# Kernel tuning notes

Hardware: AMD Instinct MI355X
Metric: run time of the kernel (lower is better)

Reference implementation:

```python
import jax, jax.numpy as jnp
import numpy as np

B, N, M, LDIM, RDIM, AGG = 4, 512, 512, 512, 512, 256


def setup_inputs() -> dict:
    key = jax.random.key(0)
    ks = jax.random.split(key, 7)
    data = jax.random.normal(ks[0], (B, N, LDIM), dtype=jnp.float32)
    crit = jax.random.normal(ks[1], (B, M, RDIM), dtype=jnp.float32)
    Wl = jax.random.normal(ks[2], (LDIM, AGG), dtype=jnp.float32) / np.sqrt(LDIM)
    bl = jax.random.normal(ks[3], (AGG,), dtype=jnp.float32) * 0.01
    Wr = jax.random.normal(ks[4], (RDIM, AGG), dtype=jnp.float32) / np.sqrt(RDIM)
    br = jax.random.normal(ks[5], (AGG,), dtype=jnp.float32) * 0.01
    agg = jax.random.uniform(ks[6], (AGG,), dtype=jnp.float32, minval=-0.01, maxval=0.01)
    return {"data": data, "crit": crit, "Wl": Wl, "bl": bl, "Wr": Wr, "br": br, "agg": agg}


def reference(data, crit, Wl, bl, Wr, br, agg):
    # linear projections
    datalin = jnp.einsum('bnl,la->bna', data, Wl) + bl   # [B,N,A]
    critlin = jnp.einsum('bmr,ra->bma', crit, Wr) + br   # [B,M,A]
    # broadcast add -> tanh -> reduce with agg vector: [B,N,M]
    linsum = jnp.tanh(datalin[:, :, None, :] + critlin[:, None, :, :])  # [B,N,M,A]
    dists = jnp.einsum('bnma,a->bnm', linsum, agg)
    return dists
```

## Files before the change

### kernel.cpp

```cpp
#include <hip/hip_runtime.h>


#define A_DIM 256
#define K_DIM 512
#define NROWS 2048

typedef unsigned short ushort;
typedef __attribute__((ext_vector_type(4))) unsigned short us4;
typedef __attribute__((ext_vector_type(8))) unsigned short us8;
typedef __attribute__((ext_vector_type(8))) short short8;
typedef __attribute__((ext_vector_type(4))) float f32x4;
typedef __attribute__((ext_vector_type(2))) float f32x2;

__device__ ushort g_eplanes[2 * (size_t)A_DIM * NROWS];

__device__ inline ushort f2bf(float x) {
    union { float f; unsigned u; } v; v.f = x;
    unsigned r = v.u + 0x7FFFu + ((v.u >> 16) & 1u);
    return (ushort)(r >> 16);
}
__device__ inline float bf2f(ushort h) {
    union { unsigned u; float f; } v; v.u = ((unsigned)h) << 16; return v.f;
}
__device__ inline unsigned pack2bf(float lo, float hi) {
    return (unsigned)f2bf(lo) | ((unsigned)f2bf(hi) << 16);
}
__device__ inline f32x2 fma2(f32x2 a, f32x2 b, f32x2 c) {
    return __builtin_elementwise_fma(a, b, c);
}

__global__ __launch_bounds__(256, 4) void proj_mfma_kernel(
    const float* __restrict__ data, const float* __restrict__ crit,
    const float* __restrict__ Wl, const float* __restrict__ bl,
    const float* __restrict__ Wr, const float* __restrict__ br)
{
    __shared__ ushort Ws[64][264];

    const int t   = threadIdx.x;
    const int bid = blockIdx.x;
    const int ct  = bid >> 7;
    const int rt  = bid & 127;
    const int src = rt >> 6;
    const int lr0 = (rt & 63) * 32;
    const int c0  = ct * 64;

    const float* X    = src ? crit : data;
    const float* bias = src ? br : bl;
    const float* W    = src ? Wr : Wl;
    ushort* E = g_eplanes + (size_t)src * ((size_t)A_DIM * NROWS);

    const int lane = t & 63;
    const int wid  = t >> 6;
    const int wm   = wid >> 1, wn = wid & 1;
    const int quad = lane >> 4, l16 = lane & 15;

    const float* xrow = X + (size_t)(lr0 + wm * 16 + l16) * K_DIM + quad * 8;
    const int aloc0 = wn * 32 + l16;

    const int kq = lane >> 4;
    const int aq = lane & 15;

    f32x4 acc0 = {0.f, 0.f, 0.f, 0.f}, acc1 = {0.f, 0.f, 0.f, 0.f};

    float4 pa0 = *(const float4*)(xrow);
    float4 pb0 = *(const float4*)(xrow + 4);
    float4 pa1 = *(const float4*)(xrow + 32);
    float4 pb1 = *(const float4*)(xrow + 36);

    for (int kc = 0; kc < 2; kc++) {
        __syncthreads();
        {
#pragma unroll
            for (int p = 0; p < 4; p++) {
                const int kb = wid * 64 + p * 16;
                f32x4 v[4];
#pragma unroll
                for (int j = 0; j < 4; j++)
                    v[j] = *(const f32x4*)(W + (size_t)(kc * 256 + kb + kq * 4 + j) * A_DIM
                                             + c0 + aq * 4);
#pragma unroll
                for (int ai = 0; ai < 4; ai++) {
                    us4 o;
#pragma unroll
                    for (int j = 0; j < 4; j++) o[j] = f2bf(v[j][ai]);
                    *(us4*)&Ws[aq * 4 + ai][kb + kq * 4] = o;
                }
            }
        }
        __syncthreads();

#pragma unroll
        for (int ls = 0; ls < 8; ls++) {
            const int s = kc * 8 + ls;
            float4 ca = pa0, cb = pb0;
            pa0 = pa1; pb0 = pb1;
            if (s < 14) {
                pa1 = *(const float4*)(xrow + (s + 2) * 32);
                pb1 = *(const float4*)(xrow + (s + 2) * 32 + 4);
            }
            union { short8 s8; unsigned u[4]; } af;
            af.u[0] = pack2bf(ca.x, ca.y);
            af.u[1] = pack2bf(ca.z, ca.w);
            af.u[2] = pack2bf(cb.x, cb.y);
            af.u[3] = pack2bf(cb.z, cb.w);
            short8 b0 = *(const short8*)&Ws[aloc0     ][ls * 32 + quad * 8];
            short8 b1 = *(const short8*)&Ws[aloc0 + 16][ls * 32 + quad * 8];
            acc0 = __builtin_amdgcn_mfma_f32_16x16x32_bf16(af.s8, b0, acc0, 0, 0, 0);
            acc1 = __builtin_amdgcn_mfma_f32_16x16x32_bf16(af.s8, b1, acc1, 0, 0, 0);
        }
    }

    const float c2 = 2.8853900817779268f;
    const int a_col0 = c0 + wn * 32 + l16;
    const int a_col1 = a_col0 + 16;
    const int row0   = lr0 + wm * 16 + quad * 4;
    const float bv0 = bias[a_col0], bv1 = bias[a_col1];
    us4 e0, e1;
#pragma unroll
    for (int i = 0; i < 4; i++) {
        float v0 = (acc0[i] + bv0) * c2;
        float v1 = (acc1[i] + bv1) * c2;
        v0 = fminf(fmaxf(v0, -15.f), 15.f);
        v1 = fminf(fmaxf(v1, -15.f), 15.f);
        e0[i] = f2bf(__builtin_amdgcn_exp2f(v0));
        e1[i] = f2bf(__builtin_amdgcn_exp2f(v1));
    }
    __builtin_nontemporal_store(e0, (us4*)(E + (size_t)a_col0 * NROWS + row0));
    __builtin_nontemporal_store(e1, (us4*)(E + (size_t)a_col1 * NROWS + row0));
}

__global__ __launch_bounds__(1024) void tanh_reduce_kernel(
    const float* __restrict__ agg, float* __restrict__ out)
{
    __shared__ __align__(16) float et [4][64][68];
    __shared__ __align__(16) float ect[4][64][68];
    __shared__ __align__(16) float aggs[256];

    const int t  = threadIdx.x;
    const int h  = t >> 8;
    const int u  = t & 255;
    const int m0 = blockIdx.x * 64;
    const int n0 = blockIdx.y * 64;
    const int b  = blockIdx.z;

    const size_t PLANE = (size_t)A_DIM * NROWS;
    const ushort* Ed = g_eplanes;
    const ushort* Ec = g_eplanes + PLANE;
    const int row_n = b * 512 + n0;
    const int row_m = b * 512 + m0;

    const int tx = u & 15;
    const int ty = u >> 4;

    if (t < 256) aggs[t] = 2.0f * agg[t];

    f32x2 acc2[4][2];
#pragma unroll
    for (int i = 0; i < 4; i++) { acc2[i][0] = (f32x2)0.f; acc2[i][1] = (f32x2)0.f; }
    float sagg = 0.f;

    const int aL = u >> 2;
    const int qd = u & 3;

    float (*eth)[68]  = et[h];
    float (*ecth)[68] = ect[h];

    {
        const size_t base = (size_t)(h * 64 + aL) * NROWS;
        us4 pn[4], pm[4];
#pragma unroll
        for (int r = 0; r < 4; r++) {
            pn[r] = *(const us4*)(Ed + base + row_n + qd * 16 + r * 4);
            pm[r] = *(const us4*)(Ec + base + row_m + qd * 16 + r * 4);
        }
#pragma unroll
        for (int r = 0; r < 4; r++) {
            float4 ev, cv;
            ev.x = bf2f(pn[r][0]); ev.y = bf2f(pn[r][1]);
            ev.z = bf2f(pn[r][2]); ev.w = bf2f(pn[r][3]);
            cv.x = bf2f(pm[r][0]); cv.y = bf2f(pm[r][1]);
            cv.z = bf2f(pm[r][2]); cv.w = bf2f(pm[r][3]);
            *(float4*)&eth [aL][qd * 16 + r * 4] = ev;
            *(float4*)&ecth[aL][qd * 16 + r * 4] = cv;
        }
    }
    __syncthreads();

    for (int qg = 0; qg < 16; qg++) {
        const float4 ag = *(const float4*)&aggs[h * 64 + qg * 4];
        sagg += (ag.x + ag.y) + (ag.z + ag.w);
        float  en[4][4];
        f32x2  fm[4][2];
#pragma unroll
        for (int v = 0; v < 4; v++) {
            float4 e4 = *(const float4*)&eth [qg * 4 + v][ty * 4];
            float4 f4 = *(const float4*)&ecth[qg * 4 + v][tx * 4];
            en[v][0] = e4.x; en[v][1] = e4.y; en[v][2] = e4.z; en[v][3] = e4.w;
            fm[v][0] = f32x2{f4.x, f4.y};
            fm[v][1] = f32x2{f4.z, f4.w};
        }
#pragma unroll
        for (int i = 0; i < 4; i++)
#pragma unroll
            for (int jp = 0; jp < 2; jp++) {
                const f32x2 one = (f32x2)1.f;
                f32x2 q0 = fma2((f32x2)en[0][i], fm[0][jp], one);
                f32x2 q1 = fma2((f32x2)en[1][i], fm[1][jp], one);
                f32x2 q2 = fma2((f32x2)en[2][i], fm[2][jp], one);
                f32x2 q3 = fma2((f32x2)en[3][i], fm[3][jp], one);
                f32x2 q01 = q0 * q1, q23 = q2 * q3;
                f32x2 n01 = fma2((f32x2)ag.x, q1, (f32x2)ag.y * q0);
                f32x2 n23 = fma2((f32x2)ag.z, q3, (f32x2)ag.w * q2);
                f32x2 N   = fma2(n01, q23, n23 * q01);
                f32x2 D   = q01 * q23;
                f32x2 r;
                r.x = __builtin_amdgcn_rcpf(D.x);
                r.y = __builtin_amdgcn_rcpf(D.y);
                acc2[i][jp] = fma2(N, r, acc2[i][jp]);
            }
    }

    const float base = 0.5f * sagg;
    float* xb = (float*)ect;
    __syncthreads();
    if (h != 0) {
        float* w = xb + ((size_t)(h - 1) * 256 + u) * 17;
#pragma unroll
        for (int i = 0; i < 4; i++)
#pragma unroll
            for (int jp = 0; jp < 2; jp++) {
                w[i * 4 + jp * 2 + 0] = base - acc2[i][jp].x;
                w[i * 4 + jp * 2 + 1] = base - acc2[i][jp].y;
            }
    }
    __syncthreads();
    if (h == 0) {
        const float* x1 = xb + (size_t)u * 17;
        const float* x2 = xb + ((size_t)256 + u) * 17;
        const float* x3 = xb + ((size_t)512 + u) * 17;
#pragma unroll
        for (int i = 0; i < 4; i++) {
            f32x4 v;
            v.x = ((base - acc2[i][0].x) + x1[i * 4 + 0]) + (x2[i * 4 + 0] + x3[i * 4 + 0]);
            v.y = ((base - acc2[i][0].y) + x1[i * 4 + 1]) + (x2[i * 4 + 1] + x3[i * 4 + 1]);
            v.z = ((base - acc2[i][1].x) + x1[i * 4 + 2]) + (x2[i * 4 + 2] + x3[i * 4 + 2]);
            v.w = ((base - acc2[i][1].y) + x1[i * 4 + 3]) + (x2[i * 4 + 3] + x3[i * 4 + 3]);
            __builtin_nontemporal_store(v,
                (f32x4*)(out + ((size_t)(b * 512 + n0 + ty * 4 + i) * 512) + m0 + tx * 4));
        }
    }
}

extern "C" void kernel_launch(void* const* d_in, const int* in_sizes, int n_in,
                              void* d_out, int out_size, void* d_ws, size_t ws_size,
                              hipStream_t stream) {
    const float* data = (const float*)d_in[0];
    const float* crit = (const float*)d_in[1];
    const float* Wl   = (const float*)d_in[2];
    const float* bl   = (const float*)d_in[3];
    const float* Wr   = (const float*)d_in[4];
    const float* br   = (const float*)d_in[5];
    const float* agg  = (const float*)d_in[6];
    float* out = (float*)d_out;

    (void)d_ws; (void)ws_size;

    proj_mfma_kernel<<<dim3(512), 256, 0, stream>>>(data, crit, Wl, bl, Wr, br);

    tanh_reduce_kernel<<<dim3(8, 8, 4), 1024, 0, stream>>>(agg, out);
}
```

Baseline: 105.7 us.

## Use 8x8 register tiles with bf16 LDS staging in tanh reduce kernel

The block drops from 1024 to 256 threads, and each thread now computes an 8x8 output tile instead of 4x4, so LDS loads are reused more per FMA. The exp planes stay in LDS as bf16, with a padded row layout and a rotated write order to spread bank accesses, and are converted to fp32 at read time. This halves the LDS footprint, and the reduction buffer is placed in a union with the staging arrays. In exchange, each thread needs many more registers (64 accumulator floats), there are fewer waves per block for latency hiding, and conversion ALU work is added in the inner loop.

```diff
diff --git a/kernel.cpp b/kernel.cpp
--- a/kernel.cpp
+++ b/kernel.cpp
@@ -129,16 +129,18 @@
     __builtin_nontemporal_store(e1, (us4*)(E + (size_t)a_col1 * NROWS + row0));
 }
 
-__global__ __launch_bounds__(1024) void tanh_reduce_kernel(
+__global__ __launch_bounds__(256) void tanh_reduce_kernel(
     const float* __restrict__ agg, float* __restrict__ out)
 {
-    __shared__ __align__(16) float et [4][64][68];
-    __shared__ __align__(16) float ect[4][64][68];
+    __shared__ __align__(16) union {
+        struct { ushort et[4][64][72]; ushort ect[4][64][72]; } p;
+        float xb[3 * 64 * 65];
+    } sm;
     __shared__ __align__(16) float aggs[256];
 
     const int t  = threadIdx.x;
-    const int h  = t >> 8;
-    const int u  = t & 255;
+    const int h  = t >> 6;
+    const int u  = t & 63;
     const int m0 = blockIdx.x * 64;
     const int n0 = blockIdx.y * 64;
     const int b  = blockIdx.z;
@@ -149,60 +151,58 @@
     const int row_n = b * 512 + n0;
     const int row_m = b * 512 + m0;
 
-    const int tx = u & 15;
-    const int ty = u >> 4;
+    const int tx = u & 7;
+    const int ty = u >> 3;
 
     if (t < 256) aggs[t] = 2.0f * agg[t];
 
-    f32x2 acc2[4][2];
-#pragma unroll
-    for (int i = 0; i < 4; i++) { acc2[i][0] = (f32x2)0.f; acc2[i][1] = (f32x2)0.f; }
+    {
+        const ushort* srcN = Ed + (size_t)(h * 64 + u) * NROWS + row_n;
+        const ushort* srcM = Ec + (size_t)(h * 64 + u) * NROWS + row_m;
+        const int key = (u >> 3) & 7;
+        us8 bn[8], bm[8];
+#pragma unroll
+        for (int ii = 0; ii < 8; ii++) {
+            const int c = ((ii + key) & 7) * 8;
+            bn[ii] = *(const us8*)(srcN + c);
+            bm[ii] = *(const us8*)(srcM + c);
+        }
+#pragma unroll
+        for (int ii = 0; ii < 8; ii++) {
+            const int c = ((ii + key) & 7) * 8;
+            *(us8*)&sm.p.et [h][u][c] = bn[ii];
+            *(us8*)&sm.p.ect[h][u][c] = bm[ii];
+        }
+    }
+
+    f32x2 acc2[8][4];
+#pragma unroll
+    for (int i = 0; i < 8; i++)
+#pragma unroll
+        for (int jp = 0; jp < 4; jp++) acc2[i][jp] = (f32x2)0.f;
     float sagg = 0.f;
 
-    const int aL = u >> 2;
-    const int qd = u & 3;
-
-    float (*eth)[68]  = et[h];
-    float (*ecth)[68] = ect[h];
-
-    {
-        const size_t base = (size_t)(h * 64 + aL) * NROWS;
-        us4 pn[4], pm[4];
-#pragma unroll
-        for (int r = 0; r < 4; r++) {
-            pn[r] = *(const us4*)(Ed + base + row_n + qd * 16 + r * 4);
-            pm[r] = *(const us4*)(Ec + base + row_m + qd * 16 + r * 4);
-        }
-#pragma unroll
-        for (int r = 0; r < 4; r++) {
-            float4 ev, cv;
-            ev.x = bf2f(pn[r][0]); ev.y = bf2f(pn[r][1]);
-            ev.z = bf2f(pn[r][2]); ev.w = bf2f(pn[r][3]);
-            cv.x = bf2f(pm[r][0]); cv.y = bf2f(pm[r][1]);
-            cv.z = bf2f(pm[r][2]); cv.w = bf2f(pm[r][3]);
-            *(float4*)&eth [aL][qd * 16 + r * 4] = ev;
-            *(float4*)&ecth[aL][qd * 16 + r * 4] = cv;
-        }
-    }
     __syncthreads();
 
     for (int qg = 0; qg < 16; qg++) {
         const float4 ag = *(const float4*)&aggs[h * 64 + qg * 4];
         sagg += (ag.x + ag.y) + (ag.z + ag.w);
-        float  en[4][4];
-        f32x2  fm[4][2];
+        float en[4][8];
+        f32x2 fm[4][4];
 #pragma unroll
         for (int v = 0; v < 4; v++) {
-            float4 e4 = *(const float4*)&eth [qg * 4 + v][ty * 4];
-            float4 f4 = *(const float4*)&ecth[qg * 4 + v][tx * 4];
-            en[v][0] = e4.x; en[v][1] = e4.y; en[v][2] = e4.z; en[v][3] = e4.w;
-            fm[v][0] = f32x2{f4.x, f4.y};
-            fm[v][1] = f32x2{f4.z, f4.w};
-        }
-#pragma unroll
-        for (int i = 0; i < 4; i++)
-#pragma unroll
-            for (int jp = 0; jp < 2; jp++) {
+            us8 e8 = *(const us8*)&sm.p.et [h][qg * 4 + v][ty * 8];
+            us8 f8 = *(const us8*)&sm.p.ect[h][qg * 4 + v][tx * 8];
+#pragma unroll
+            for (int j = 0; j < 8; j++) en[v][j] = bf2f(e8[j]);
+#pragma unroll
+            for (int jp = 0; jp < 4; jp++)
+                fm[v][jp] = f32x2{bf2f(f8[jp * 2]), bf2f(f8[jp * 2 + 1])};
+        }
+#pragma unroll
+        for (int i = 0; i < 8; i++)
+#pragma unroll
+            for (int jp = 0; jp < 4; jp++) {
                 const f32x2 one = (f32x2)1.f;
                 f32x2 q0 = fma2((f32x2)en[0][i], fm[0][jp], one);
                 f32x2 q1 = fma2((f32x2)en[1][i], fm[1][jp], one);
@@ -221,32 +221,35 @@
     }
 
     const float base = 0.5f * sagg;
-    float* xb = (float*)ect;
     __syncthreads();
     if (h != 0) {
-        float* w = xb + ((size_t)(h - 1) * 256 + u) * 17;
-#pragma unroll
-        for (int i = 0; i < 4; i++)
-#pragma unroll
-            for (int jp = 0; jp < 2; jp++) {
-                w[i * 4 + jp * 2 + 0] = base - acc2[i][jp].x;
-                w[i * 4 + jp * 2 + 1] = base - acc2[i][jp].y;
+        float* w = sm.xb + ((size_t)(h - 1) * 64 + u) * 65;
+#pragma unroll
+        for (int i = 0; i < 8; i++)
+#pragma unroll
+            for (int jp = 0; jp < 4; jp++) {
+                w[i * 8 + jp * 2 + 0] = base - acc2[i][jp].x;
+                w[i * 8 + jp * 2 + 1] = base - acc2[i][jp].y;
             }
     }
     __syncthreads();
     if (h == 0) {
-        const float* x1 = xb + (size_t)u * 17;
-        const float* x2 = xb + ((size_t)256 + u) * 17;
-        const float* x3 = xb + ((size_t)512 + u) * 17;
-#pragma unroll
-        for (int i = 0; i < 4; i++) {
-            f32x4 v;
-            v.x = ((base - acc2[i][0].x) + x1[i * 4 + 0]) + (x2[i * 4 + 0] + x3[i * 4 + 0]);
-            v.y = ((base - acc2[i][0].y) + x1[i * 4 + 1]) + (x2[i * 4 + 1] + x3[i * 4 + 1]);
-            v.z = ((base - acc2[i][1].x) + x1[i * 4 + 2]) + (x2[i * 4 + 2] + x3[i * 4 + 2]);
-            v.w = ((base - acc2[i][1].y) + x1[i * 4 + 3]) + (x2[i * 4 + 3] + x3[i * 4 + 3]);
-            __builtin_nontemporal_store(v,
-                (f32x4*)(out + ((size_t)(b * 512 + n0 + ty * 4 + i) * 512) + m0 + tx * 4));
+        const float* x1 = sm.xb + (size_t)u * 65;
+        const float* x2 = sm.xb + ((size_t)64 + u) * 65;
+        const float* x3 = sm.xb + ((size_t)128 + u) * 65;
+#pragma unroll
+        for (int i = 0; i < 8; i++) {
+            float r[8];
+#pragma unroll
+            for (int jp = 0; jp < 4; jp++) {
+                const int k0 = i * 8 + jp * 2;
+                r[jp * 2 + 0] = ((base - acc2[i][jp].x) + x1[k0 + 0]) + (x2[k0 + 0] + x3[k0 + 0]);
+                r[jp * 2 + 1] = ((base - acc2[i][jp].y) + x1[k0 + 1]) + (x2[k0 + 1] + x3[k0 + 1]);
+            }
+            f32x4 v0 = {r[0], r[1], r[2], r[3]}, v1 = {r[4], r[5], r[6], r[7]};
+            float* orow = out + (size_t)(b * 512 + n0 + ty * 8 + i) * 512 + m0 + tx * 8;
+            __builtin_nontemporal_store(v0, (f32x4*)orow);
+            __builtin_nontemporal_store(v1, (f32x4*)(orow + 4));
         }
     }
 }
@@ -267,5 +270,5 @@
 
     proj_mfma_kernel<<<dim3(512), 256, 0, stream>>>(data, crit, Wl, bl, Wr, br);
 
-    tanh_reduce_kernel<<<dim3(8, 8, 4), 1024, 0, stream>>>(agg, out);
-}
+    tanh_reduce_kernel<<<dim3(8, 8, 4), 256, 0, stream>>>(agg, out);
+}
```

Measured after the change: 112.0 us. +5.9%, slower.
